# Kernel optimization log

Hardware: AMD Instinct MI355X
Metric: run time of the kernel (lower is better)

Reference implementation:

```python
import jax, jax.numpy as jnp
import numpy as np

N, E = 50000, 800000
IN, HID, HEADS, OUT = 128, 64, 4, 32


def _lin_init(key, fin, fout):
    k1, k2 = jax.random.split(key)
    W = jax.random.normal(k1, (fin, fout), jnp.float32) / np.float32(np.sqrt(fin))
    b = jax.random.normal(k2, (fout,), jnp.float32) * 0.01
    return W, b


def setup_inputs() -> dict:
    key = jax.random.key(0)
    ks = jax.random.split(key, 12)
    x = jax.random.normal(ks[0], (N, IN), jnp.float32)
    edge_index = jax.random.randint(ks[1], (2, E), 0, N, dtype=jnp.int32)
    Wq1, bq1 = _lin_init(ks[2], IN, HEADS * HID)
    Wk1, bk1 = _lin_init(ks[3], IN, HEADS * HID)
    Wv1, bv1 = _lin_init(ks[4], IN, HEADS * HID)
    Ws1, bs1 = _lin_init(ks[5], IN, HID)  # skip: concat=False -> in -> hidden
    Wq2, bq2 = _lin_init(ks[6], HID, HEADS * HID)
    Wk2, bk2 = _lin_init(ks[7], HID, HEADS * HID)
    Wv2, bv2 = _lin_init(ks[8], HID, HEADS * HID)
    Ws2, bs2 = _lin_init(ks[9], HID, HID)
    ln_g = jnp.ones((HID,), jnp.float32)
    ln_b = jnp.zeros((HID,), jnp.float32)
    Wf, bf = _lin_init(ks[10], HID, OUT)
    return dict(x=x, edge_index=edge_index,
                Wq1=Wq1, bq1=bq1, Wk1=Wk1, bk1=bk1, Wv1=Wv1, bv1=bv1, Ws1=Ws1, bs1=bs1,
                Wq2=Wq2, bq2=bq2, Wk2=Wk2, bk2=bk2, Wv2=Wv2, bv2=bv2, Ws2=Ws2, bs2=bs2,
                ln_g=ln_g, ln_b=ln_b, Wf=Wf, bf=bf)


def transformer_conv(x, src, dst, Wq, bq, Wk, bk, Wv, bv, Ws, bs):
    """PyG TransformerConv, heads=HEADS, concat=False (head-mean), root_weight=True."""
    n = x.shape[0]
    q = (x @ Wq + bq).reshape(n, HEADS, HID)
    k = (x @ Wk + bk).reshape(n, HEADS, HID)
    v = (x @ Wv + bv).reshape(n, HEADS, HID)
    # per-edge attention logits: query at target (dst), key at source (src)
    logits = jnp.einsum('ehd,ehd->eh', q[dst], k[src]) / np.float32(np.sqrt(HID))  # [E,H]
    m = jax.ops.segment_max(logits, dst, num_segments=n)          # [N,H]
    e = jnp.exp(logits - m[dst])
    s = jax.ops.segment_sum(e, dst, num_segments=n)               # [N,H]
    alpha = e / s[dst]                                            # segment softmax
    agg = jax.ops.segment_sum(alpha[:, :, None] * v[src], dst, num_segments=n)  # [N,H,D]
    return agg.mean(axis=1) + (x @ Ws + bs)


def layernorm(x, g, b):
    mu = x.mean(-1, keepdims=True)
    var = x.var(-1, keepdims=True)
    return (x - mu) / jnp.sqrt(var + 1e-5) * g + b


def reference(x, edge_index, Wq1, bq1, Wk1, bk1, Wv1, bv1, Ws1, bs1,
              Wq2, bq2, Wk2, bk2, Wv2, bv2, Ws2, bs2, ln_g, ln_b, Wf, bf):
    src, dst = edge_index[0], edge_index[1]
    h = transformer_conv(x, src, dst, Wq1, bq1, Wk1, bk1, Wv1, bv1, Ws1, bs1)
    h = jax.nn.relu(layernorm(h, ln_g, ln_b))  # dropout = identity (eval)
    h = transformer_conv(h, src, dst, Wq2, bq2, Wk2, bk2, Wv2, bv2, Ws2, bs2)
    h = layernorm(h, ln_g, ln_b)  # k == num_layers-2: no relu/dropout
    return h @ Wf + bf
```

## Files before the change

### kernel.cpp

```cpp
#include <hip/hip_runtime.h>
#include <hip/hip_fp16.h>
#include <math.h>

#define NN 50000
#define EE 800000
#define HEADS 4
#define HIDD 64
#define OUTF 32

struct __align__(8) h4v { __half2 a, b; };

template<int KDIM>
__global__ __launch_bounds__(256) void qkvs_gemm(
    const float* __restrict__ X,
    const float* __restrict__ Wq, const float* __restrict__ bq,
    const float* __restrict__ Wk, const float* __restrict__ bk,
    const float* __restrict__ Wv, const float* __restrict__ bv,
    const float* __restrict__ Ws, const float* __restrict__ bs,
    float* __restrict__ Q, __half* __restrict__ KV, float* __restrict__ SKP)
{
    const int nt = blockIdx.x;
    const float* W; const float* bias; int mode, bcol, wstride;
    if (nt < 4)       { W = Wq; bias = bq; mode = 0; bcol = nt*64;     wstride = 256; }
    else if (nt < 8)  { W = Wk; bias = bk; mode = 1; bcol = (nt-4)*64; wstride = 256; }
    else if (nt < 12) { W = Wv; bias = bv; mode = 2; bcol = (nt-8)*64; wstride = 256; }
    else              { W = Ws; bias = bs; mode = 3; bcol = 0;         wstride = 64;  }

    __shared__ float sAT[32][68];
    __shared__ float sB[32][64];

    const int tid = threadIdx.x;
    const int tx = tid & 15, ty = tid >> 4;
    const int row0 = blockIdx.y * 64;

    float acc[4][4] = {};

    for (int k0 = 0; k0 < KDIM; k0 += 32) {
        #pragma unroll
        for (int i = 0; i < 2; ++i) {
            int li = tid + 256*i;
            int r = li >> 3, c = li & 7;
            int gr = row0 + r;
            float4 a4 = {0.f,0.f,0.f,0.f};
            if (gr < NN) a4 = *(const float4*)&X[(size_t)gr*KDIM + k0 + c*4];
            sAT[c*4+0][r] = a4.x; sAT[c*4+1][r] = a4.y;
            sAT[c*4+2][r] = a4.z; sAT[c*4+3][r] = a4.w;
        }
        #pragma unroll
        for (int i = 0; i < 2; ++i) {
            int li = tid + 256*i;
            int kk = li >> 4, c4 = li & 15;
            *(float4*)&sB[kk][c4*4] =
                *(const float4*)&W[(size_t)(k0+kk)*wstride + bcol + c4*4];
        }
        __syncthreads();
        #pragma unroll
        for (int kk = 0; kk < 32; ++kk) {
            float4 a4 = *(const float4*)&sAT[kk][ty*4];
            float4 b4 = *(const float4*)&sB[kk][tx*4];
            float a[4] = {a4.x, a4.y, a4.z, a4.w};
            float b[4] = {b4.x, b4.y, b4.z, b4.w};
            #pragma unroll
            for (int i = 0; i < 4; ++i)
                #pragma unroll
                for (int j = 0; j < 4; ++j)
                    acc[i][j] += a[i]*b[j];
        }
        __syncthreads();
    }
    #pragma unroll
    for (int i = 0; i < 4; ++i) {
        int gr = row0 + ty*4 + i;
        if (gr >= NN) continue;
        float o[4];
        #pragma unroll
        for (int j = 0; j < 4; ++j) o[j] = acc[i][j] + bias[bcol + tx*4 + j];
        if (mode == 0) {
            *(float4*)&Q[(size_t)gr*256 + bcol + tx*4] = {o[0],o[1],o[2],o[3]};
        } else if (mode == 3) {
            *(float4*)&SKP[(size_t)gr*64 + tx*4] = {o[0],o[1],o[2],o[3]};
        } else {
            h4v hh;
            hh.a = __floats2half2_rn(o[0], o[1]);
            hh.b = __floats2half2_rn(o[2], o[3]);
            size_t base = (size_t)gr*512 + (mode == 2 ? 256 : 0) + bcol + tx*4;
            *(h4v*)&KV[base] = hh;
        }
    }
}

__global__ __launch_bounds__(256) void hist_kernel(const int* __restrict__ dstA,
                                                   int* __restrict__ deg)
{
    int e = blockIdx.x * 256 + threadIdx.x;
    atomicAdd(&deg[dstA[e]], 1);
}

__global__ __launch_bounds__(1024) void scan_kernel(const int* __restrict__ deg,
                                                    int* __restrict__ rowptr,
                                                    int* __restrict__ cursor)
{
    __shared__ int sdata[1024];
    __shared__ int soff;
    const int tid = threadIdx.x;
    if (tid == 0) soff = 0;
    __syncthreads();
    for (int base = 0; base < NN; base += 1024) {
        int v = (base + tid < NN) ? deg[base + tid] : 0;
        sdata[tid] = v;
        __syncthreads();
        #pragma unroll
        for (int off = 1; off < 1024; off <<= 1) {
            int t = (tid >= off) ? sdata[tid - off] : 0;
            __syncthreads();
            sdata[tid] += t;
            __syncthreads();
        }
        int excl = sdata[tid] - v;
        if (base + tid < NN) {
            rowptr[base + tid] = soff + excl;
            cursor[base + tid] = soff + excl;
        }
        int total = sdata[1023];
        __syncthreads();
        if (tid == 0) soff += total;
        __syncthreads();
    }
    if (tid == 0) rowptr[NN] = EE;
}

__global__ __launch_bounds__(256) void scatter_kernel(const int* __restrict__ srcA,
                                                      const int* __restrict__ dstA,
                                                      int* __restrict__ cursor,
                                                      int* __restrict__ colidx)
{
    int e = blockIdx.x * 256 + threadIdx.x;
    int p = atomicAdd(&cursor[dstA[e]], 1);
    colidx[p] = srcA[e];
}

template<bool RELU>
__global__ __launch_bounds__(256) void node_attn(
    const int* __restrict__ rowptr, const int* __restrict__ colidx,
    const float* __restrict__ Q, const __half* __restrict__ KV,
    const float* __restrict__ SKP,
    const float* __restrict__ g, const float* __restrict__ b,
    float* __restrict__ Hout)
{
    int n = (blockIdx.x * blockDim.x + threadIdx.x) >> 6;
    if (n >= NN) return;
    const int lane = threadIdx.x & 63;
    const int h = lane >> 4, t = lane & 15;
    const int hoff = h*64 + t*4;

    const float4 q4 = *(const float4*)&Q[(size_t)n*256 + hoff];

    float4 acc = {0.f,0.f,0.f,0.f};
    float ssum = 0.f;
    const int e0 = rowptr[n], e1 = rowptr[n+1];
    int e = e0;
    for (; e + 2 <= e1; e += 2) {
        const int s0 = colidx[e], s1 = colidx[e+1];
        const size_t b0 = (size_t)s0*512 + hoff;
        const size_t b1 = (size_t)s1*512 + hoff;
        const h4v kh0 = *(const h4v*)&KV[b0];
        const h4v kh1 = *(const h4v*)&KV[b1];
        const h4v vh0 = *(const h4v*)&KV[b0 + 256];
        const h4v vh1 = *(const h4v*)&KV[b1 + 256];
        const float2 k0a = __half22float2(kh0.a), k0b = __half22float2(kh0.b);
        const float2 k1a = __half22float2(kh1.a), k1b = __half22float2(kh1.b);
        float p0 = q4.x*k0a.x + q4.y*k0a.y + q4.z*k0b.x + q4.w*k0b.y;
        float p1 = q4.x*k1a.x + q4.y*k1a.y + q4.z*k1b.x + q4.w*k1b.y;
        p0 += __shfl_xor(p0, 1);  p1 += __shfl_xor(p1, 1);
        p0 += __shfl_xor(p0, 2);  p1 += __shfl_xor(p1, 2);
        p0 += __shfl_xor(p0, 4);  p1 += __shfl_xor(p1, 4);
        p0 += __shfl_xor(p0, 8);  p1 += __shfl_xor(p1, 8);
        const float eh0 = expf(p0 * 0.125f);
        const float eh1 = expf(p1 * 0.125f);
        const float2 v0a = __half22float2(vh0.a), v0b = __half22float2(vh0.b);
        const float2 v1a = __half22float2(vh1.a), v1b = __half22float2(vh1.b);
        ssum  += eh0 + eh1;
        acc.x += eh0*v0a.x + eh1*v1a.x;
        acc.y += eh0*v0a.y + eh1*v1a.y;
        acc.z += eh0*v0b.x + eh1*v1b.x;
        acc.w += eh0*v0b.y + eh1*v1b.y;
    }
    for (; e < e1; ++e) {
        const int s = colidx[e];
        const size_t b0 = (size_t)s*512 + hoff;
        const h4v kh = *(const h4v*)&KV[b0];
        const h4v vh = *(const h4v*)&KV[b0 + 256];
        const float2 ka = __half22float2(kh.a), kb = __half22float2(kh.b);
        float p = q4.x*ka.x + q4.y*ka.y + q4.z*kb.x + q4.w*kb.y;
        p += __shfl_xor(p, 1);
        p += __shfl_xor(p, 2);
        p += __shfl_xor(p, 4);
        p += __shfl_xor(p, 8);
        const float eh = expf(p * 0.125f);
        const float2 va = __half22float2(vh.a), vb = __half22float2(vh.b);
        ssum  += eh;
        acc.x += eh*va.x; acc.y += eh*va.y; acc.z += eh*vb.x; acc.w += eh*vb.y;
    }
    const float inv = (ssum != 0.f) ? 1.f/ssum : 0.f;
    acc.x *= inv; acc.y *= inv; acc.z *= inv; acc.w *= inv;

    #pragma unroll
    for (int o = 16; o < 64; o <<= 1) {
        acc.x += __shfl_xor(acc.x, o); acc.y += __shfl_xor(acc.y, o);
        acc.z += __shfl_xor(acc.z, o); acc.w += __shfl_xor(acc.w, o);
    }
    const float4 sk4 = *(const float4*)&SKP[(size_t)n*64 + t*4];
    float4 val;
    val.x = acc.x*0.25f + sk4.x; val.y = acc.y*0.25f + sk4.y;
    val.z = acc.z*0.25f + sk4.z; val.w = acc.w*0.25f + sk4.w;

    float m  = val.x + val.y + val.z + val.w;
    float m2 = val.x*val.x + val.y*val.y + val.z*val.z + val.w*val.w;
    #pragma unroll
    for (int o = 1; o < 16; o <<= 1) { m += __shfl_xor(m, o); m2 += __shfl_xor(m2, o); }
    m *= (1.f/64.f); m2 *= (1.f/64.f);
    const float rstd = rsqrtf(m2 - m*m + 1e-5f);
    const float4 g4 = *(const float4*)&g[t*4];
    const float4 b4 = *(const float4*)&b[t*4];
    float4 y;
    y.x = (val.x - m)*rstd*g4.x + b4.x;
    y.y = (val.y - m)*rstd*g4.y + b4.y;
    y.z = (val.z - m)*rstd*g4.z + b4.z;
    y.w = (val.w - m)*rstd*g4.w + b4.w;
    if (RELU) {
        y.x = fmaxf(y.x, 0.f); y.y = fmaxf(y.y, 0.f);
        y.z = fmaxf(y.z, 0.f); y.w = fmaxf(y.w, 0.f);
    }
    if (h == 0) *(float4*)&Hout[(size_t)n*64 + t*4] = y;
}

__global__ __launch_bounds__(256) void final_gemm(
    const float* __restrict__ H, const float* __restrict__ Wf,
    const float* __restrict__ bf, float* __restrict__ out)
{
    __shared__ float sW[64][32];
    __shared__ float sH[8][64];
    const int tid = threadIdx.x;
    #pragma unroll
    for (int i = 0; i < 8; ++i) {
        int li = tid + 256*i;
        sW[li >> 5][li & 31] = Wf[li];
    }
    const int n0 = blockIdx.x * 8;
    #pragma unroll
    for (int i = 0; i < 2; ++i) {
        int li = tid + 256*i;
        int r = li >> 6, d = li & 63;
        int gn = n0 + r;
        sH[r][d] = (gn < NN) ? H[(size_t)gn*64 + d] : 0.f;
    }
    __syncthreads();
    const int o = tid & 31, nl = tid >> 5;
    const int gn = n0 + nl;
    if (gn >= NN) return;
    float acc = bf[o];
    #pragma unroll
    for (int dd = 0; dd < 64; ++dd) acc += sH[nl][dd] * sW[dd][o];
    out[(size_t)gn*32 + o] = acc;
}

extern "C" void kernel_launch(void* const* d_in, const int* in_sizes, int n_in,
                              void* d_out, int out_size, void* d_ws, size_t ws_size,
                              hipStream_t stream) {
    const float* x   = (const float*)d_in[0];
    const int*   ei  = (const int*)d_in[1];
    const int* srcA = ei;
    const int* dstA = ei + EE;
    const float *Wq1=(const float*)d_in[2],  *bq1=(const float*)d_in[3];
    const float *Wk1=(const float*)d_in[4],  *bk1=(const float*)d_in[5];
    const float *Wv1=(const float*)d_in[6],  *bv1=(const float*)d_in[7];
    const float *Ws1=(const float*)d_in[8],  *bs1=(const float*)d_in[9];
    const float *Wq2=(const float*)d_in[10], *bq2=(const float*)d_in[11];
    const float *Wk2=(const float*)d_in[12], *bk2=(const float*)d_in[13];
    const float *Wv2=(const float*)d_in[14], *bv2=(const float*)d_in[15];
    const float *Ws2=(const float*)d_in[16], *bs2=(const float*)d_in[17];
    const float *ln_g=(const float*)d_in[18],*ln_b=(const float*)d_in[19];
    const float *Wf=(const float*)d_in[20],  *bf=(const float*)d_in[21];
    float* out = (float*)d_out;

    float* ws = (float*)d_ws;
    size_t off = 0;
    float* Q    = ws + off; off += (size_t)NN*256;
    __half* KV  = (__half*)(ws + off); off += (size_t)NN*256;
    float* SKP  = ws + off; off += (size_t)NN*64;
    float* H1   = ws + off; off += (size_t)NN*64;
    float* H2   = ws + off; off += (size_t)NN*64;
    int* deg    = (int*)(ws + off); off += NN;
    int* rowptr = (int*)(ws + off); off += NN + 1;
    int* cursor = (int*)(ws + off); off += NN;
    int* colidx = (int*)(ws + off); off += EE;

    const dim3 gemmGrid(13, (NN + 63) / 64);
    const int edgeBlocks = EE / 256;
    const int nodeBlocks = NN / 4;

    hipMemsetAsync(deg, 0, NN * sizeof(int), stream);
    hist_kernel<<<edgeBlocks, 256, 0, stream>>>(dstA, deg);
    scan_kernel<<<1, 1024, 0, stream>>>(deg, rowptr, cursor);
    scatter_kernel<<<edgeBlocks, 256, 0, stream>>>(srcA, dstA, cursor, colidx);

    qkvs_gemm<128><<<gemmGrid, 256, 0, stream>>>(x, Wq1,bq1, Wk1,bk1, Wv1,bv1, Ws1,bs1,
                                                 Q, KV, SKP);
    node_attn<true><<<nodeBlocks, 256, 0, stream>>>(rowptr, colidx, Q, KV, SKP,
                                                    ln_g, ln_b, H1);

    qkvs_gemm<64><<<gemmGrid, 256, 0, stream>>>(H1, Wq2,bq2, Wk2,bk2, Wv2,bv2, Ws2,bs2,
                                                Q, KV, SKP);
    node_attn<false><<<nodeBlocks, 256, 0, stream>>>(rowptr, colidx, Q, KV, SKP,
                                                     ln_g, ln_b, H2);

    final_gemm<<<NN / 8, 256, 0, stream>>>(H2, Wf, bf, out);
}
```

Before: 753.9 us.

## Interleave K/V per lane, enlarge GEMM row tile, remap blocks for XCD locality

The K and V halves are now stored interleaved per head and lane, so the attention kernel fetches one 16-byte vector per edge instead of two 8-byte loads from separate locations. The QKVS GEMM tile grows from 64 to 128 rows, giving each thread 8x4 outputs, and uses a 1D grid remapped so consecutive work items land on the same XCD for L2 reuse of the X rows. The attention kernel also switches to fast __expf. The costs are more registers per GEMM thread and slightly lower precision in the exponent.

```diff
diff --git a/kernel.cpp b/kernel.cpp
--- a/kernel.cpp
+++ b/kernel.cpp
@@ -7,8 +7,10 @@
 #define HEADS 4
 #define HIDD 64
 #define OUTF 32
-
-struct __align__(8) h4v { __half2 a, b; };
+#define NXCD 8
+
+struct __align__(8)  h4v { __half2 a, b; };
+struct __align__(16) h8v { __half2 a, b, c, d; };
 
 template<int KDIM>
 __global__ __launch_bounds__(256) void qkvs_gemm(
@@ -19,26 +21,33 @@
     const float* __restrict__ Ws, const float* __restrict__ bs,
     float* __restrict__ Q, __half* __restrict__ KV, float* __restrict__ SKP)
 {
-    const int nt = blockIdx.x;
+    const int nwg = gridDim.x;
+    const int i   = blockIdx.x;
+    const int q8  = nwg >> 3, r8 = nwg & 7;
+    const int xcd = i & 7, j = i >> 3;
+    const int w   = (xcd < r8 ? xcd * (q8 + 1) : r8 * (q8 + 1) + (xcd - r8) * q8) + j;
+
+    const int nt   = w % 13;
+    const int row0 = (w / 13) * 128;
+
     const float* W; const float* bias; int mode, bcol, wstride;
     if (nt < 4)       { W = Wq; bias = bq; mode = 0; bcol = nt*64;     wstride = 256; }
     else if (nt < 8)  { W = Wk; bias = bk; mode = 1; bcol = (nt-4)*64; wstride = 256; }
     else if (nt < 12) { W = Wv; bias = bv; mode = 2; bcol = (nt-8)*64; wstride = 256; }
     else              { W = Ws; bias = bs; mode = 3; bcol = 0;         wstride = 64;  }
 
-    __shared__ float sAT[32][68];
+    __shared__ float sAT[32][132];
     __shared__ float sB[32][64];
 
     const int tid = threadIdx.x;
     const int tx = tid & 15, ty = tid >> 4;
-    const int row0 = blockIdx.y * 64;
-
-    float acc[4][4] = {};
+
+    float acc[8][4] = {};
 
     for (int k0 = 0; k0 < KDIM; k0 += 32) {
         #pragma unroll
-        for (int i = 0; i < 2; ++i) {
-            int li = tid + 256*i;
+        for (int it = 0; it < 4; ++it) {
+            int li = tid + 256*it;
             int r = li >> 3, c = li & 7;
             int gr = row0 + r;
             float4 a4 = {0.f,0.f,0.f,0.f};
@@ -47,8 +56,8 @@
             sAT[c*4+2][r] = a4.z; sAT[c*4+3][r] = a4.w;
         }
         #pragma unroll
-        for (int i = 0; i < 2; ++i) {
-            int li = tid + 256*i;
+        for (int it = 0; it < 2; ++it) {
+            int li = tid + 256*it;
             int kk = li >> 4, c4 = li & 15;
             *(float4*)&sB[kk][c4*4] =
                 *(const float4*)&W[(size_t)(k0+kk)*wstride + bcol + c4*4];
@@ -56,34 +65,37 @@
         __syncthreads();
         #pragma unroll
         for (int kk = 0; kk < 32; ++kk) {
-            float4 a4 = *(const float4*)&sAT[kk][ty*4];
+            float4 a0 = *(const float4*)&sAT[kk][ty*8];
+            float4 a1 = *(const float4*)&sAT[kk][ty*8+4];
             float4 b4 = *(const float4*)&sB[kk][tx*4];
-            float a[4] = {a4.x, a4.y, a4.z, a4.w};
-            float b[4] = {b4.x, b4.y, b4.z, b4.w};
+            float a[8] = {a0.x,a0.y,a0.z,a0.w, a1.x,a1.y,a1.z,a1.w};
+            float b[4] = {b4.x,b4.y,b4.z,b4.w};
             #pragma unroll
-            for (int i = 0; i < 4; ++i)
+            for (int ii = 0; ii < 8; ++ii)
                 #pragma unroll
-                for (int j = 0; j < 4; ++j)
-                    acc[i][j] += a[i]*b[j];
-        }
-        __syncthreads();
-    }
-    #pragma unroll
-    for (int i = 0; i < 4; ++i) {
-        int gr = row0 + ty*4 + i;
+                for (int jj = 0; jj < 4; ++jj)
+                    acc[ii][jj] += a[ii]*b[jj];
+        }
+        __syncthreads();
+    }
+
+    const float4 bia = *(const float4*)&bias[bcol + tx*4];
+    #pragma unroll
+    for (int ii = 0; ii < 8; ++ii) {
+        int gr = row0 + ty*8 + ii;
         if (gr >= NN) continue;
-        float o[4];
-        #pragma unroll
-        for (int j = 0; j < 4; ++j) o[j] = acc[i][j] + bias[bcol + tx*4 + j];
+        float o0 = acc[ii][0] + bia.x, o1 = acc[ii][1] + bia.y;
+        float o2 = acc[ii][2] + bia.z, o3 = acc[ii][3] + bia.w;
         if (mode == 0) {
-            *(float4*)&Q[(size_t)gr*256 + bcol + tx*4] = {o[0],o[1],o[2],o[3]};
+            *(float4*)&Q[(size_t)gr*256 + bcol + tx*4] = {o0,o1,o2,o3};
         } else if (mode == 3) {
-            *(float4*)&SKP[(size_t)gr*64 + tx*4] = {o[0],o[1],o[2],o[3]};
+            *(float4*)&SKP[(size_t)gr*64 + tx*4] = {o0,o1,o2,o3};
         } else {
             h4v hh;
-            hh.a = __floats2half2_rn(o[0], o[1]);
-            hh.b = __floats2half2_rn(o[2], o[3]);
-            size_t base = (size_t)gr*512 + (mode == 2 ? 256 : 0) + bcol + tx*4;
+            hh.a = __floats2half2_rn(o0, o1);
+            hh.b = __floats2half2_rn(o2, o3);
+            int h = (mode == 1) ? nt-4 : nt-8;
+            size_t base = (size_t)gr*512 + h*128 + tx*8 + (mode == 2 ? 4 : 0);
             *(h4v*)&KV[base] = hh;
         }
     }
@@ -151,9 +163,9 @@
     if (n >= NN) return;
     const int lane = threadIdx.x & 63;
     const int h = lane >> 4, t = lane & 15;
-    const int hoff = h*64 + t*4;
-
-    const float4 q4 = *(const float4*)&Q[(size_t)n*256 + hoff];
+    const int kvoff = h*128 + t*8;
+
+    const float4 q4 = *(const float4*)&Q[(size_t)n*256 + h*64 + t*4];
 
     float4 acc = {0.f,0.f,0.f,0.f};
     float ssum = 0.f;
@@ -161,24 +173,20 @@
     int e = e0;
     for (; e + 2 <= e1; e += 2) {
         const int s0 = colidx[e], s1 = colidx[e+1];
-        const size_t b0 = (size_t)s0*512 + hoff;
-        const size_t b1 = (size_t)s1*512 + hoff;
-        const h4v kh0 = *(const h4v*)&KV[b0];
-        const h4v kh1 = *(const h4v*)&KV[b1];
-        const h4v vh0 = *(const h4v*)&KV[b0 + 256];
-        const h4v vh1 = *(const h4v*)&KV[b1 + 256];
-        const float2 k0a = __half22float2(kh0.a), k0b = __half22float2(kh0.b);
-        const float2 k1a = __half22float2(kh1.a), k1b = __half22float2(kh1.b);
+        const h8v kv0 = *(const h8v*)&KV[(size_t)s0*512 + kvoff];
+        const h8v kv1 = *(const h8v*)&KV[(size_t)s1*512 + kvoff];
+        const float2 k0a = __half22float2(kv0.a), k0b = __half22float2(kv0.b);
+        const float2 k1a = __half22float2(kv1.a), k1b = __half22float2(kv1.b);
         float p0 = q4.x*k0a.x + q4.y*k0a.y + q4.z*k0b.x + q4.w*k0b.y;
         float p1 = q4.x*k1a.x + q4.y*k1a.y + q4.z*k1b.x + q4.w*k1b.y;
         p0 += __shfl_xor(p0, 1);  p1 += __shfl_xor(p1, 1);
         p0 += __shfl_xor(p0, 2);  p1 += __shfl_xor(p1, 2);
         p0 += __shfl_xor(p0, 4);  p1 += __shfl_xor(p1, 4);
         p0 += __shfl_xor(p0, 8);  p1 += __shfl_xor(p1, 8);
-        const float eh0 = expf(p0 * 0.125f);
-        const float eh1 = expf(p1 * 0.125f);
-        const float2 v0a = __half22float2(vh0.a), v0b = __half22float2(vh0.b);
-        const float2 v1a = __half22float2(vh1.a), v1b = __half22float2(vh1.b);
+        const float eh0 = __expf(p0 * 0.125f);
+        const float eh1 = __expf(p1 * 0.125f);
+        const float2 v0a = __half22float2(kv0.c), v0b = __half22float2(kv0.d);
+        const float2 v1a = __half22float2(kv1.c), v1b = __half22float2(kv1.d);
         ssum  += eh0 + eh1;
         acc.x += eh0*v0a.x + eh1*v1a.x;
         acc.y += eh0*v0a.y + eh1*v1a.y;
@@ -187,17 +195,15 @@
     }
     for (; e < e1; ++e) {
         const int s = colidx[e];
-        const size_t b0 = (size_t)s*512 + hoff;
-        const h4v kh = *(const h4v*)&KV[b0];
-        const h4v vh = *(const h4v*)&KV[b0 + 256];
-        const float2 ka = __half22float2(kh.a), kb = __half22float2(kh.b);
+        const h8v kv = *(const h8v*)&KV[(size_t)s*512 + kvoff];
+        const float2 ka = __half22float2(kv.a), kb = __half22float2(kv.b);
         float p = q4.x*ka.x + q4.y*ka.y + q4.z*kb.x + q4.w*kb.y;
         p += __shfl_xor(p, 1);
         p += __shfl_xor(p, 2);
         p += __shfl_xor(p, 4);
         p += __shfl_xor(p, 8);
-        const float eh = expf(p * 0.125f);
-        const float2 va = __half22float2(vh.a), vb = __half22float2(vh.b);
+        const float eh = __expf(p * 0.125f);
+        const float2 va = __half22float2(kv.c), vb = __half22float2(kv.d);
         ssum  += eh;
         acc.x += eh*va.x; acc.y += eh*va.y; acc.z += eh*vb.x; acc.w += eh*vb.y;
     }
@@ -295,7 +301,8 @@
     int* cursor = (int*)(ws + off); off += NN;
     int* colidx = (int*)(ws + off); off += EE;
 
-    const dim3 gemmGrid(13, (NN + 63) / 64);
+    const int rowTiles  = (NN + 127) / 128;
+    const int gemmGrid  = 13 * rowTiles;
     const int edgeBlocks = EE / 256;
     const int nodeBlocks = NN / 4;
 
```

Result: no change. 743.2 us (-1.4%).
